# Kernel tuning notes

Hardware: AMD Instinct MI355X
Metric: run time of the kernel (lower is better)

## Reference

```python
import jax, jax.numpy as jnp
import numpy as np

EPS = 1e-5


def layer_norm(x, g, b):
    mu = jnp.mean(x, axis=-1, keepdims=True)
    var = jnp.var(x, axis=-1, keepdims=True)
    return (x - mu) * jax.lax.rsqrt(var + EPS) * g + b


def setup_inputs() -> dict:
    key = jax.random.key(0)
    ks = jax.random.split(key, 10)
    B, N, D, H, DFF = 4, 2048, 384, 6, 2048
    s = lambda fan: 1.0 / np.sqrt(fan)
    return {
        "x": jax.random.normal(ks[0], (B, N, D), dtype=jnp.float32),
        "norm_g": jnp.ones((D,), jnp.float32),
        "norm_b": jnp.zeros((D,), jnp.float32),
        "w_qkv": jax.random.uniform(ks[1], (D, 3 * D), jnp.float32, -s(D), s(D)),
        "b_qkv": jax.random.uniform(ks[2], (3 * D,), jnp.float32, -s(D), s(D)),
        "w1": jax.random.uniform(ks[3], (D, DFF), jnp.float32, -s(D), s(D)),
        "b1": jax.random.uniform(ks[4], (DFF,), jnp.float32, -s(D), s(D)),
        "w2": jax.random.uniform(ks[5], (DFF, D), jnp.float32, -s(DFF), s(DFF)),
        "b2": jax.random.uniform(ks[6], (D,), jnp.float32, -s(DFF), s(DFF)),
    }


def reference(x, norm_g, norm_b, w_qkv, b_qkv, w1, b1, w2, b2):
    H = 6
    B, N, D = x.shape
    hd = D // H
    scale = hd ** -0.5

    # --- attention (pre-norm, shared LayerNorm params) ---
    out = layer_norm(x, norm_g, norm_b)
    qkv = out @ w_qkv + b_qkv                     # [B, N, 3D]
    q, k, v = jnp.split(qkv, 3, axis=-1)
    to_heads = lambda t: t.reshape(B, N, H, hd).transpose(0, 2, 1, 3)  # b h n d
    q, k, v = to_heads(q), to_heads(k), to_heads(v)
    scores = jnp.einsum('bhid,bhjd->bhij', q, k) * scale
    attn = jax.nn.softmax(scores, axis=-1)        # dropout is identity in eval
    att = jnp.einsum('bhij,bhjd->bhid', attn, v)  # [B, H, N, hd]
    att = att.transpose(0, 2, 1, 3).reshape(B, N, D)
    x2 = x + att

    # --- MLP (same shared LayerNorm) ---
    y = layer_norm(x2, norm_g, norm_b)
    h = jax.nn.gelu(y @ w1 + b1, approximate=False)  # torch F.gelu exact
    mlp = h @ w2 + b2
    return x2 + mlp
```

## Files before the change

### kernel.cpp

```cpp
#include <hip/hip_runtime.h>
#include <cstdint>
#include <cstddef>

#define DEV static __device__ __forceinline__

typedef __attribute__((ext_vector_type(8))) short short8;
typedef __attribute__((ext_vector_type(4))) float f32x4;
typedef __attribute__((ext_vector_type(16))) float f32x16;
typedef __attribute__((ext_vector_type(4))) unsigned short u16x4;
typedef __attribute__((ext_vector_type(2))) unsigned short u16x2;

constexpr int kB = 4, kN = 2048, kD = 384, kH = 6, kDFF = 2048;
constexpr int kM = kB * kN;
constexpr int kBH = kB * kH;
constexpr float kQPre = 0.18033688011112042f;

DEV float exp2fast(float f) { return __builtin_amdgcn_exp2f(f); }

DEV unsigned short f2b(float f) {
  union { float fp; uint32_t u; } v; v.fp = f;
  return (unsigned short)((v.u + 0x7fffu + ((v.u >> 16) & 1u)) >> 16);
}

DEV void gload16(const unsigned short* g, unsigned short* l) {
  __builtin_amdgcn_global_load_lds(
      (const __attribute__((address_space(1))) unsigned int*)g,
      (__attribute__((address_space(3))) unsigned int*)l, 16, 0, 0);
}

DEV float gelu_fast(float x) {
  float t = exp2fast(x * (2.3022081f + 0.1029432f * x * x));
  return x - x * __builtin_amdgcn_rcpf(t + 1.0f);
}

__global__ __launch_bounds__(256) void k_pre(
    const float* __restrict__ wqkv, unsigned short* __restrict__ wqkvT,
    const float* __restrict__ w1,   unsigned short* __restrict__ w1T,
    const float* __restrict__ w2,   unsigned short* __restrict__ w2T,
    const float* __restrict__ x, const float* __restrict__ g,
    const float* __restrict__ bta, unsigned short* __restrict__ y) {
  const int tid = threadIdx.x;
  if (blockIdx.x >= 492) {
    int row  = (blockIdx.x - 492) * 4 + (tid >> 6);
    int lane = tid & 63;
    const float* xr = x + (size_t)row * kD;
    float4 a = *(const float4*)(xr + lane * 4);
    float2 c = *(const float2*)(xr + 256 + lane * 2);
    float s  = a.x + a.y + a.z + a.w + c.x + c.y;
    float ss = a.x*a.x + a.y*a.y + a.z*a.z + a.w*a.w + c.x*c.x + c.y*c.y;
#pragma unroll
    for (int m = 1; m < 64; m <<= 1) {
      s  += __shfl_xor(s,  m, 64);
      ss += __shfl_xor(ss, m, 64);
    }
    float mean = s * (1.0f / kD);
    float var  = ss * (1.0f / kD) - mean * mean;
    float r = rsqrtf(var + 1e-5f);
    float4 g4 = *(const float4*)(g + lane * 4);
    float2 g2 = *(const float2*)(g + 256 + lane * 2);
    float4 b4 = *(const float4*)(bta + lane * 4);
    float2 b2 = *(const float2*)(bta + 256 + lane * 2);
    unsigned short* yr = y + (size_t)row * kD;
    u16x4 o4;
    o4[0] = f2b((a.x - mean) * r * g4.x + b4.x);
    o4[1] = f2b((a.y - mean) * r * g4.y + b4.y);
    o4[2] = f2b((a.z - mean) * r * g4.z + b4.z);
    o4[3] = f2b((a.w - mean) * r * g4.w + b4.w);
    *(u16x4*)(yr + lane * 4) = o4;
    u16x2 o2;
    o2[0] = f2b((c.x - mean) * r * g2.x + b2.x);
    o2[1] = f2b((c.y - mean) * r * g2.y + b2.y);
    *(u16x2*)(yr + 256 + lane * 2) = o2;
    return;
  }
  __shared__ unsigned short t[64][66];
  int idx = blockIdx.x;
  const float* w; unsigned short* wT; int K, Nn, nbk;
  if (idx < 108)      { w = wqkv; wT = wqkvT; K = 384;  Nn = 1152; nbk = 6; }
  else if (idx < 300) { w = w1;   wT = w1T;   K = 384;  Nn = 2048; nbk = 6;  idx -= 108; }
  else                { w = w2;   wT = w2T;   K = 2048; Nn = 384;  nbk = 32; idx -= 300; }
  const int bk = idx % nbk, bn = idx / nbk;
  const int k0 = bk << 6, n0 = bn << 6;
  const int cl = tid & 63, rw = tid >> 6;
#pragma unroll
  for (int it = 0; it < 16; ++it) {
    int kk = it * 4 + rw;
    t[cl][kk] = f2b(w[(size_t)(k0 + kk) * Nn + n0 + cl]);
  }
  __syncthreads();
  const int kq = (tid & 15) << 2;
  const int nr = tid >> 4;
#pragma unroll
  for (int it = 0; it < 4; ++it) {
    int nn = it * 16 + nr;
    u16x4 v;
    v[0] = t[nn][kq]; v[1] = t[nn][kq + 1]; v[2] = t[nn][kq + 2]; v[3] = t[nn][kq + 3];
    *(u16x4*)&wT[(size_t)(n0 + nn) * K + k0 + kq] = v;
  }
}

__global__ __launch_bounds__(256) void k_layernorm(
    const float* __restrict__ x, const float* __restrict__ g,
    const float* __restrict__ bta, unsigned short* __restrict__ y) {
  int row  = blockIdx.x * 4 + (threadIdx.x >> 6);
  int lane = threadIdx.x & 63;
  const float* xr = x + (size_t)row * kD;
  float4 a = *(const float4*)(xr + lane * 4);
  float2 c = *(const float2*)(xr + 256 + lane * 2);
  float s  = a.x + a.y + a.z + a.w + c.x + c.y;
  float ss = a.x*a.x + a.y*a.y + a.z*a.z + a.w*a.w + c.x*c.x + c.y*c.y;
#pragma unroll
  for (int m = 1; m < 64; m <<= 1) {
    s  += __shfl_xor(s,  m, 64);
    ss += __shfl_xor(ss, m, 64);
  }
  float mean = s * (1.0f / kD);
  float var  = ss * (1.0f / kD) - mean * mean;
  float r = rsqrtf(var + 1e-5f);
  float4 g4 = *(const float4*)(g + lane * 4);
  float2 g2 = *(const float2*)(g + 256 + lane * 2);
  float4 b4 = *(const float4*)(bta + lane * 4);
  float2 b2 = *(const float2*)(bta + 256 + lane * 2);
  unsigned short* yr = y + (size_t)row * kD;
  u16x4 o4;
  o4[0] = f2b((a.x - mean) * r * g4.x + b4.x);
  o4[1] = f2b((a.y - mean) * r * g4.y + b4.y);
  o4[2] = f2b((a.z - mean) * r * g4.z + b4.z);
  o4[3] = f2b((a.w - mean) * r * g4.w + b4.w);
  *(u16x4*)(yr + lane * 4) = o4;
  u16x2 o2;
  o2[0] = f2b((c.x - mean) * r * g2.x + b2.x);
  o2[1] = f2b((c.y - mean) * r * g2.y + b2.y);
  *(u16x2*)(yr + 256 + lane * 2) = o2;
}

template <int MODE, int TM>
__global__ __launch_bounds__(256) void k_gemm(
    const unsigned short* __restrict__ A, const unsigned short* __restrict__ Bt,
    const float* __restrict__ bias, int K, int Nn, int nbm,
    unsigned short* __restrict__ oq, unsigned short* __restrict__ okk,
    unsigned short* __restrict__ ov, unsigned short* __restrict__ oh,
    const float* __restrict__ res, float* __restrict__ out) {
  constexpr int FI = (TM >= 64) ? TM / 64 : 1;
  constexpr int FJ = (TM >= 64) ? 2 : 1;
  __shared__ unsigned short lA[2][TM * 32];
  __shared__ unsigned short lB[2][128 * 32];
  const int tid = threadIdx.x, wid = tid >> 6, lane = tid & 63;
  const int bm = blockIdx.x % nbm, bn = blockIdx.x / nbm;
  const int m0 = bm * TM, n0 = bn * 128;
  const int wr = (TM >= 64) ? (wid >> 1) : 0;
  const int wc = (TM >= 64) ? (wid & 1) : wid;
  const int wmo = wr * (TM >> 1);
  const int wno = wc * (FJ * 32);
  const int l31 = lane & 31, lh = lane >> 5;
  const int gsw = (l31 >> 1) & 3;

  f32x16 acc[FI][FJ];
#pragma unroll
  for (int i = 0; i < FI; i++)
#pragma unroll
    for (int j = 0; j < FJ; j++)
#pragma unroll
      for (int r = 0; r < 16; r++) acc[i][j][r] = 0.f;

  const int srow = (lane >> 2);
  const int scc  = (lane & 3) << 3;

  auto stage = [&](int buf, int k0) {
    if constexpr (TM >= 64) {
#pragma unroll
      for (int p = 0; p < TM / 64; p++) {
        int row = ((wid + (p << 2)) << 4) + srow;
        int sl  = ((lane & 3) ^ ((row >> 1) & 3)) << 3;
        gload16(A + (size_t)(m0 + row) * K + k0 + sl, &lA[buf][(row << 5) + scc]);
      }
    } else {
      if (tid < TM * 4) {
        int row = tid >> 2;
        int sl  = ((tid & 3) ^ ((row >> 1) & 3)) << 3;
        gload16(A + (size_t)(m0 + row) * K + k0 + sl,
                &lA[buf][(row << 5) + ((tid & 3) << 3)]);
      }
    }
#pragma unroll
    for (int p = 0; p < 2; p++) {
      int row = ((wid + (p << 2)) << 4) + srow;
      int sl  = ((lane & 3) ^ ((row >> 1) & 3)) << 3;
      gload16(Bt + (size_t)(n0 + row) * K + k0 + sl, &lB[buf][(row << 5) + scc]);
    }
  };

  stage(0, 0);

  const int nkt = K >> 5;
  for (int kt = 0; kt < nkt; ++kt) {
    const int cur = kt & 1;
    __syncthreads();
    if (kt + 1 < nkt) stage(cur ^ 1, (kt + 1) << 5);
    short8 af[FI][2], bf[FJ][2];
#pragma unroll
    for (int i = 0; i < FI; i++)
#pragma unroll
      for (int ks = 0; ks < 2; ks++)
        af[i][ks] = *(const short8*)&lA[cur][(wmo + (i << 5) + l31) * 32 +
                                            ((((ks << 1) + lh) ^ gsw) << 3)];
#pragma unroll
    for (int j = 0; j < FJ; j++)
#pragma unroll
      for (int ks = 0; ks < 2; ks++)
        bf[j][ks] = *(const short8*)&lB[cur][(wno + (j << 5) + l31) * 32 +
                                            ((((ks << 1) + lh) ^ gsw) << 3)];
#pragma unroll
    for (int i = 0; i < FI; i++)
#pragma unroll
      for (int j = 0; j < FJ; j++)
#pragma unroll
        for (int ks = 0; ks < 2; ks++)
          acc[i][j] = __builtin_amdgcn_mfma_f32_32x32x16_bf16(af[i][ks], bf[j][ks],
                                                              acc[i][j], 0, 0, 0);
  }

#pragma unroll
  for (int i = 0; i < FI; i++) {
#pragma unroll
    for (int j = 0; j < FJ; j++) {
      int col = n0 + wno + (j << 5) + l31;
      float bv = bias[col];
#pragma unroll
      for (int reg = 0; reg < 16; ++reg) {
        int m = m0 + wmo + (i << 5) + (reg & 3) + ((reg >> 2) << 3) + (lh << 2);
        float cvl = acc[i][j][reg] + bv;
        if (MODE == 0) {
          int bI = m >> 11, nI = m & 2047;
          if (col < 384) {
            int hh = col >> 6, dd = col & 63;
            oq[(((size_t)bI * kH + hh) * kN + nI) * 64 + dd] = f2b(cvl * kQPre);
          } else if (col < 768) {
            int c2 = col - 384; int hh = c2 >> 6, dd = c2 & 63;
            okk[(((size_t)bI * kH + hh) * kN + nI) * 64 + dd] = f2b(cvl);
          } else {
            int c2 = col - 768; int hh = c2 >> 6, dd = c2 & 63;
            ov[(((size_t)bI * kH + hh) * 64 + dd) * kN + nI] = f2b(cvl);
          }
        } else if (MODE == 1) {
          oh[(size_t)m * kDFF + col] = f2b(gelu_fast(cvl));
        } else {
          size_t idx = (size_t)m * kD + col;
          out[idx] = res[idx] + cvl;
        }
      }
    }
  }
}

__global__ __launch_bounds__(256) void k_attn(
    const unsigned short* __restrict__ Q, const unsigned short* __restrict__ Kg,
    const unsigned short* __restrict__ Vt, const float* __restrict__ x,
    float* __restrict__ x2) {
  __shared__ unsigned short lK[2][64 * 64];
  __shared__ unsigned short lV[2][64 * 64];
  __shared__ unsigned short lP[4][32 * 64];
  const int tid = threadIdx.x, wid = tid >> 6, lane = tid & 63;
  const int swz = (blockIdx.x & 7) * (gridDim.x >> 3) + (blockIdx.x >> 3);
  const int bh = swz >> 5, qt = swz & 31;
  const int b = bh / kH, h = bh - b * kH;
  const unsigned short* Qp = Q  + (size_t)bh * kN * 64;
  const unsigned short* Kp = Kg + (size_t)bh * kN * 64;
  const unsigned short* Vp = Vt + (size_t)bh * 64 * kN;
  const int l31 = lane & 31, lh = lane >> 5;
  const int qh = wid & 1, kvh = wid >> 1;
  const int q0 = qt * 64;
  const int psw = l31 & 7;

  const int sr  = ((wid << 3) + (lane >> 3));
  const int scc = (lane & 7) << 3;

  short8 qb[4];
#pragma unroll
  for (int ks = 0; ks < 4; ++ks)
    qb[ks] = *(const short8*)(Qp + (size_t)(q0 + qh * 32 + l31) * 64 + ks * 16 + lh * 8);

  const short8 ones = {0x3F80, 0x3F80, 0x3F80, 0x3F80, 0x3F80, 0x3F80, 0x3F80, 0x3F80};
  f32x16 o[2], ol;
#pragma unroll
  for (int db = 0; db < 2; ++db)
#pragma unroll
    for (int r = 0; r < 16; r++) o[db][r] = 0.f;
#pragma unroll
  for (int r = 0; r < 16; r++) ol[r] = 0.f;

  auto stage = [&](int buf, int t) {
#pragma unroll
    for (int p = 0; p < 2; p++) {
      int r = sr + (p << 5);
      int sl = ((lane & 7) ^ (r & 7)) << 3;
      gload16(Kp + (size_t)(t * 64 + r) * 64 + sl, &lK[buf][(r << 6) + scc]);
      gload16(Vp + (size_t)r * kN + t * 64 + sl,   &lV[buf][(r << 6) + scc]);
    }
  };

  stage(0, 0);

  constexpr int kNT = kN / 64;
  for (int t = 0; t < kNT; ++t) {
    const int cur = t & 1;
    __syncthreads();
    if (t + 1 < kNT) stage(cur ^ 1, t + 1);

    f32x16 s;
#pragma unroll
    for (int r = 0; r < 16; r++) s[r] = 0.f;
#pragma unroll
    for (int ks = 0; ks < 4; ++ks) {
      int krow = kvh * 32 + l31;
      short8 kf = *(const short8*)&lK[cur][(krow << 6) +
                                          ((((ks << 1) + lh) ^ psw) << 3)];
      s = __builtin_amdgcn_mfma_f32_32x32x16_bf16(kf, qb[ks], s, 0, 0, 0);
    }

#pragma unroll
    for (int g = 0; g < 4; ++g) {
      float p0 = exp2fast(s[4 * g + 0]);
      float p1 = exp2fast(s[4 * g + 1]);
      float p2 = exp2fast(s[4 * g + 2]);
      float p3 = exp2fast(s[4 * g + 3]);
      uint32_t w0, w1;
      asm("v_cvt_pk_bf16_f32 %0, %1, %2" : "=v"(w0) : "v"(p0), "v"(p1));
      asm("v_cvt_pk_bf16_f32 %0, %1, %2" : "=v"(w1) : "v"(p2), "v"(p3));
      uint2 wv; wv.x = w0; wv.y = w1;
      *(uint2*)&lP[wid][(l31 << 6) + ((g ^ psw) << 3) + (lh << 2)] = wv;
    }

    short8 pa[2];
#pragma unroll
    for (int ks = 0; ks < 2; ++ks)
      pa[ks] = *(const short8*)&lP[wid][(l31 << 6) + ((((ks << 1) + lh) ^ psw) << 3)];
#pragma unroll
    for (int ks = 0; ks < 2; ++ks)
      ol = __builtin_amdgcn_mfma_f32_32x32x16_bf16(pa[ks], ones, ol, 0, 0, 0);
#pragma unroll
    for (int db = 0; db < 2; ++db) {
      int vrow = db * 32 + l31;
#pragma unroll
      for (int ks = 0; ks < 2; ++ks) {
        short8 vb = *(const short8*)&lV[cur][(vrow << 6) +
                      ((((kvh << 2) + (ks << 1) + lh) ^ (vrow & 7)) << 3)];
        o[db] = __builtin_amdgcn_mfma_f32_32x32x16_bf16(pa[ks], vb, o[db], 0, 0, 0);
      }
    }
  }

  __syncthreads();
  float* fb = (float*)&lP[0][0] + qh * 2048;
  float* lb = (float*)&lK[0][0] + qh * 32;
  if (kvh == 1) {
#pragma unroll
    for (int reg = 0; reg < 16; ++reg) {
      int row = (reg & 3) + ((reg >> 2) << 3) + (lh << 2);
      fb[row * 64 +      l31] = o[0][reg];
      fb[row * 64 + 32 + l31] = o[1][reg];
      if (l31 == 0) lb[row] = ol[reg];
    }
  }
  __syncthreads();
  if (kvh == 0) {
#pragma unroll
    for (int reg = 0; reg < 16; ++reg) {
      int row = (reg & 3) + ((reg >> 2) << 3) + (lh << 2);
      float inv = __builtin_amdgcn_rcpf(ol[reg] + lb[row]);
      int gq = q0 + qh * 32 + row;
#pragma unroll
      for (int db = 0; db < 2; ++db) {
        float val = o[db][reg] + fb[row * 64 + db * 32 + l31];
        size_t idx = ((size_t)(b * kN + gq)) * kD + h * 64 + db * 32 + l31;
        x2[idx] = x[idx] + val * inv;
      }
    }
  }
}

extern "C" void kernel_launch(void* const* d_in, const int* in_sizes, int n_in,
                              void* d_out, int out_size, void* d_ws, size_t ws_size,
                              hipStream_t stream) {
  const float* x    = (const float*)d_in[0];
  const float* ng   = (const float*)d_in[1];
  const float* nb   = (const float*)d_in[2];
  const float* wqkv = (const float*)d_in[3];
  const float* bqkv = (const float*)d_in[4];
  const float* w1   = (const float*)d_in[5];
  const float* b1   = (const float*)d_in[6];
  const float* w2   = (const float*)d_in[7];
  const float* b2   = (const float*)d_in[8];
  float* out = (float*)d_out;

  char* p = (char*)d_ws;
  auto take = [&](size_t bytes) -> char* {
    char* r = p; p += (bytes + 255) & ~(size_t)255; return r;
  };
  unsigned short* y     = (unsigned short*)take((size_t)kM * kD * 2);
  unsigned short* wqkvT = (unsigned short*)take((size_t)3 * kD * kD * 2);
  unsigned short* w1T   = (unsigned short*)take((size_t)kDFF * kD * 2);
  unsigned short* w2T   = (unsigned short*)take((size_t)kD * kDFF * 2);
  unsigned short* Qw    = (unsigned short*)take((size_t)kM * kD * 2);
  unsigned short* Kw    = (unsigned short*)take((size_t)kM * kD * 2);
  unsigned short* Vtw   = (unsigned short*)take((size_t)kM * kD * 2);
  float*          x2    = (float*)take((size_t)kM * kD * 4);
  unsigned short* hbuf  = (unsigned short*)take((size_t)kM * kDFF * 2);

  k_pre<<<492 + kM / 4, 256, 0, stream>>>(wqkv, wqkvT, w1, w1T, w2, w2T,
                                          x, ng, nb, y);
  k_gemm<0, 64><<<128 * 9, 256, 0, stream>>>(y, wqkvT, bqkv, kD, 3 * kD, 128,
                                             Qw, Kw, Vtw, nullptr, nullptr, nullptr);
  k_attn<<<kBH * 32, 256, 0, stream>>>(Qw, Kw, Vtw, x, x2);
  k_layernorm<<<kM / 4, 256, 0, stream>>>(x2, ng, nb, y);
  k_gemm<1, 128><<<64 * 16, 256, 0, stream>>>(y, w1T, b1, kD, kDFF, 64,
                                              nullptr, nullptr, nullptr, hbuf, nullptr, nullptr);
  k_gemm<2, 32><<<256 * 3, 256, 0, stream>>>(hbuf, w2T, b2, kDFF, kD, 256,
                                             nullptr, nullptr, nullptr, nullptr, x2, out);
}
```

Before: 148.9 us.

## Keep softmax probabilities in registers and compute row sums with shuffles in attention

The attention kernel no longer writes the exp'd score tile to LDS and reads it back as an MFMA operand. It packs the bf16 probabilities in registers and exchanges halves across lanes with cross-lane shuffles, then computes O^T as V^T times P^T. The row sum is accumulated in fp32 with a shuffle-reduce instead of an extra MFMA against a ones vector. The epilogue reduces through a padded LDS buffer and writes the output with vectorized float4 loads and stores, adding one more barrier.

```diff
diff --git a/kernel.cpp b/kernel.cpp
--- a/kernel.cpp
+++ b/kernel.cpp
@@ -5,7 +5,6 @@
 #define DEV static __device__ __forceinline__
 
 typedef __attribute__((ext_vector_type(8))) short short8;
-typedef __attribute__((ext_vector_type(4))) float f32x4;
 typedef __attribute__((ext_vector_type(16))) float f32x16;
 typedef __attribute__((ext_vector_type(4))) unsigned short u16x4;
 typedef __attribute__((ext_vector_type(2))) unsigned short u16x2;
@@ -257,9 +256,9 @@
     const unsigned short* __restrict__ Q, const unsigned short* __restrict__ Kg,
     const unsigned short* __restrict__ Vt, const float* __restrict__ x,
     float* __restrict__ x2) {
-  __shared__ unsigned short lK[2][64 * 64];
-  __shared__ unsigned short lV[2][64 * 64];
-  __shared__ unsigned short lP[4][32 * 64];
+  __shared__ unsigned short sh[4 * 4096];
+  unsigned short* lK = sh;
+  unsigned short* lV = sh + 8192;
   const int tid = threadIdx.x, wid = tid >> 6, lane = tid & 63;
   const int swz = (blockIdx.x & 7) * (gridDim.x >> 3) + (blockIdx.x >> 3);
   const int bh = swz >> 5, qt = swz & 31;
@@ -270,7 +269,7 @@
   const int l31 = lane & 31, lh = lane >> 5;
   const int qh = wid & 1, kvh = wid >> 1;
   const int q0 = qt * 64;
-  const int psw = l31 & 7;
+  const int rsw7 = l31 & 7;
 
   const int sr  = ((wid << 3) + (lane >> 3));
   const int scc = (lane & 7) << 3;
@@ -280,22 +279,20 @@
   for (int ks = 0; ks < 4; ++ks)
     qb[ks] = *(const short8*)(Qp + (size_t)(q0 + qh * 32 + l31) * 64 + ks * 16 + lh * 8);
 
-  const short8 ones = {0x3F80, 0x3F80, 0x3F80, 0x3F80, 0x3F80, 0x3F80, 0x3F80, 0x3F80};
-  f32x16 o[2], ol;
-#pragma unroll
-  for (int db = 0; db < 2; ++db)
-#pragma unroll
-    for (int r = 0; r < 16; r++) o[db][r] = 0.f;
-#pragma unroll
-  for (int r = 0; r < 16; r++) ol[r] = 0.f;
+  f32x16 o[2];
+#pragma unroll
+  for (int dt = 0; dt < 2; ++dt)
+#pragma unroll
+    for (int r = 0; r < 16; r++) o[dt][r] = 0.f;
+  float l_r = 0.f;
 
   auto stage = [&](int buf, int t) {
 #pragma unroll
     for (int p = 0; p < 2; p++) {
       int r = sr + (p << 5);
       int sl = ((lane & 7) ^ (r & 7)) << 3;
-      gload16(Kp + (size_t)(t * 64 + r) * 64 + sl, &lK[buf][(r << 6) + scc]);
-      gload16(Vp + (size_t)r * kN + t * 64 + sl,   &lV[buf][(r << 6) + scc]);
+      gload16(Kp + (size_t)(t * 64 + r) * 64 + sl, &lK[buf * 4096 + (r << 6) + scc]);
+      gload16(Vp + (size_t)r * kN + t * 64 + sl,   &lV[buf * 4096 + (r << 6) + scc]);
     }
   };
 
@@ -312,69 +309,92 @@
     for (int r = 0; r < 16; r++) s[r] = 0.f;
 #pragma unroll
     for (int ks = 0; ks < 4; ++ks) {
-      int krow = kvh * 32 + l31;
-      short8 kf = *(const short8*)&lK[cur][(krow << 6) +
-                                          ((((ks << 1) + lh) ^ psw) << 3)];
+      short8 kf = *(const short8*)&lK[cur * 4096 + ((kvh * 32 + l31) << 6) +
+                                      ((((ks << 1) + lh) ^ rsw7) << 3)];
       s = __builtin_amdgcn_mfma_f32_32x32x16_bf16(kf, qb[ks], s, 0, 0, 0);
     }
 
+    uint32_t Aw[4], Bw[4];
+    float lsum = 0.f;
 #pragma unroll
     for (int g = 0; g < 4; ++g) {
       float p0 = exp2fast(s[4 * g + 0]);
       float p1 = exp2fast(s[4 * g + 1]);
       float p2 = exp2fast(s[4 * g + 2]);
       float p3 = exp2fast(s[4 * g + 3]);
-      uint32_t w0, w1;
-      asm("v_cvt_pk_bf16_f32 %0, %1, %2" : "=v"(w0) : "v"(p0), "v"(p1));
-      asm("v_cvt_pk_bf16_f32 %0, %1, %2" : "=v"(w1) : "v"(p2), "v"(p3));
-      uint2 wv; wv.x = w0; wv.y = w1;
-      *(uint2*)&lP[wid][(l31 << 6) + ((g ^ psw) << 3) + (lh << 2)] = wv;
-    }
-
-    short8 pa[2];
-#pragma unroll
-    for (int ks = 0; ks < 2; ++ks)
-      pa[ks] = *(const short8*)&lP[wid][(l31 << 6) + ((((ks << 1) + lh) ^ psw) << 3)];
-#pragma unroll
-    for (int ks = 0; ks < 2; ++ks)
-      ol = __builtin_amdgcn_mfma_f32_32x32x16_bf16(pa[ks], ones, ol, 0, 0, 0);
-#pragma unroll
-    for (int db = 0; db < 2; ++db) {
-      int vrow = db * 32 + l31;
+      lsum += (p0 + p1) + (p2 + p3);
+      asm("v_cvt_pk_bf16_f32 %0, %1, %2" : "=v"(Aw[g]) : "v"(p0), "v"(p1));
+      asm("v_cvt_pk_bf16_f32 %0, %1, %2" : "=v"(Bw[g]) : "v"(p2), "v"(p3));
+    }
+    l_r += lsum + __shfl_xor(lsum, 32, 64);
+
+    short8 pb[2];
+#pragma unroll
+    for (int ks = 0; ks < 2; ++ks) {
+      uint32_t cA = lh ? Aw[2 * ks + 1] : Aw[2 * ks];
+      uint32_t cB = lh ? Bw[2 * ks + 1] : Bw[2 * ks];
+      uint32_t dA = lh ? Aw[2 * ks] : Aw[2 * ks + 1];
+      uint32_t dB = lh ? Bw[2 * ks] : Bw[2 * ks + 1];
+      uint32_t sA = __shfl_xor(dA, 32, 64);
+      uint32_t sB = __shfl_xor(dB, 32, 64);
+      union { uint32_t u[4]; short8 s8; } bld;
+      bld.u[0] = lh ? sA : cA;
+      bld.u[1] = lh ? sB : cB;
+      bld.u[2] = lh ? cA : sA;
+      bld.u[3] = lh ? cB : sB;
+      pb[ks] = bld.s8;
+    }
+
+#pragma unroll
+    for (int dt = 0; dt < 2; ++dt) {
 #pragma unroll
       for (int ks = 0; ks < 2; ++ks) {
-        short8 vb = *(const short8*)&lV[cur][(vrow << 6) +
-                      ((((kvh << 2) + (ks << 1) + lh) ^ (vrow & 7)) << 3)];
-        o[db] = __builtin_amdgcn_mfma_f32_32x32x16_bf16(pa[ks], vb, o[db], 0, 0, 0);
+        short8 va = *(const short8*)&lV[cur * 4096 + (((dt << 5) + l31) << 6) +
+                        ((((kvh << 2) + (ks << 1) + lh) ^ rsw7) << 3)];
+        o[dt] = __builtin_amdgcn_mfma_f32_32x32x16_bf16(va, pb[ks], o[dt], 0, 0, 0);
       }
     }
   }
 
   __syncthreads();
-  float* fb = (float*)&lP[0][0] + qh * 2048;
-  float* lb = (float*)&lK[0][0] + qh * 32;
+  float* fb = (float*)sh;
+  float* lb = (float*)sh + 64 * 65;
+  const int q = qh * 32 + l31;
   if (kvh == 1) {
 #pragma unroll
-    for (int reg = 0; reg < 16; ++reg) {
-      int row = (reg & 3) + ((reg >> 2) << 3) + (lh << 2);
-      fb[row * 64 +      l31] = o[0][reg];
-      fb[row * 64 + 32 + l31] = o[1][reg];
-      if (l31 == 0) lb[row] = ol[reg];
-    }
+    for (int dt = 0; dt < 2; ++dt)
+#pragma unroll
+      for (int reg = 0; reg < 16; ++reg) {
+        int d = (dt << 5) + (reg & 3) + ((reg >> 2) << 3) + (lh << 2);
+        fb[q * 65 + d] = o[dt][reg];
+      }
+    if (lh == 0) lb[q] = l_r;
   }
   __syncthreads();
   if (kvh == 0) {
 #pragma unroll
-    for (int reg = 0; reg < 16; ++reg) {
-      int row = (reg & 3) + ((reg >> 2) << 3) + (lh << 2);
-      float inv = __builtin_amdgcn_rcpf(ol[reg] + lb[row]);
-      int gq = q0 + qh * 32 + row;
-#pragma unroll
-      for (int db = 0; db < 2; ++db) {
-        float val = o[db][reg] + fb[row * 64 + db * 32 + l31];
-        size_t idx = ((size_t)(b * kN + gq)) * kD + h * 64 + db * 32 + l31;
-        x2[idx] = x[idx] + val * inv;
-      }
+    for (int dt = 0; dt < 2; ++dt)
+#pragma unroll
+      for (int reg = 0; reg < 16; ++reg) {
+        int d = (dt << 5) + (reg & 3) + ((reg >> 2) << 3) + (lh << 2);
+        fb[q * 65 + d] += o[dt][reg];
+      }
+    if (lh == 0) lb[q] += l_r;
+  }
+  __syncthreads();
+  {
+    int row = tid >> 2, dc = (tid & 3) << 4;
+    float inv = __builtin_amdgcn_rcpf(lb[row]);
+    size_t base = ((size_t)(b * kN + q0 + row)) * kD + h * 64 + dc;
+#pragma unroll
+    for (int i = 0; i < 16; i += 4) {
+      float4 xv = *(const float4*)(x + base + i);
+      float4 ov;
+      ov.x = xv.x + fb[row * 65 + dc + i + 0] * inv;
+      ov.y = xv.y + fb[row * 65 + dc + i + 1] * inv;
+      ov.z = xv.z + fb[row * 65 + dc + i + 2] * inv;
+      ov.w = xv.w + fb[row * 65 + dc + i + 3] * inv;
+      *(float4*)(x2 + base + i) = ov;
     }
   }
 }
```

Measured after the change: 148.4 us. About the same (-0.3%).
